# Kernel tuning notes

Hardware: AMD Instinct MI355X
Metric: run time of the kernel (lower is better)

## Reference

```python
import jax, jax.numpy as jnp
import numpy as np

N = 100000   # num entities / tail rows
D_IN = 128
D_OUT = 128
R = 8        # num relations
E = 131072   # edges per relation
B = 32768    # head entities per relation


def setup_inputs() -> dict:
    key = jax.random.key(0)
    ks = jax.random.split(key, 8)
    x = jax.random.normal(ks[0], (N, D_IN), dtype=jnp.float32)
    tail_rep = jax.random.normal(ks[1], (N, D_IN), dtype=jnp.float32)
    # Linear(in, out, bias=False) weight: [out, in], xavier-ish scale
    W = jax.random.normal(ks[2], (D_OUT, D_IN), dtype=jnp.float32) * (1.414 / np.sqrt(D_IN))
    # match_matrix embedding -> per-relation [in, out] matrices
    rel_W = jax.random.normal(ks[3], (R, D_IN, D_OUT), dtype=jnp.float32) * (1.0 / np.sqrt(D_IN))
    edge_weights = jax.random.uniform(ks[4], (R, E), dtype=jnp.float32)
    edge_rows = jax.random.randint(ks[5], (R, E), 0, B, dtype=jnp.int32)
    edge_cols = jax.random.randint(ks[6], (R, E), 0, N, dtype=jnp.int32)
    # head_indice: unique global entity ids per relation (torch code assigns by index)
    rng = np.random.default_rng(0)
    head = np.stack([rng.choice(N, size=B, replace=False) for _ in range(R)]).astype(np.int32)
    head_indice = jnp.asarray(head)
    return {"x": x, "tail_rep": tail_rep, "W": W, "rel_W": rel_W,
            "edge_weights": edge_weights, "edge_rows": edge_rows,
            "edge_cols": edge_cols, "head_indice": head_indice}


def reference(x, tail_rep, W, rel_W, edge_weights, edge_rows, edge_cols, head_indice):
    # emb_all = original_map(input)
    emb_all = x @ W.T                                   # [N, D_OUT]
    # per-relation dense transform of all tails: tail_rep @ rel_W[r]
    transformed = jnp.einsum('ni,rio->rno', tail_rep, rel_W)   # [R, N, D_OUT]
    # sparse.mm(sp_edge_e, all_rep_h): gather tail rows per edge, weight, segment-sum by local head row
    gathered = jnp.take_along_axis(transformed, edge_cols[:, :, None], axis=1)  # [R, E, D_OUT]
    contrib = edge_weights[:, :, None] * gathered                                # [R, E, D_OUT]
    seg = lambda c, rows: jax.ops.segment_sum(c, rows, num_segments=B)
    new_rep = jax.vmap(seg)(contrib, edge_rows)                                  # [R, B, D_OUT]
    # emb_all[ent_indice] = rel_update + emb_all[ent_indice]  (per relation, sequentially) == scatter-add
    emb_all = emb_all.at[head_indice.reshape(-1)].add(new_rep.reshape(-1, D_OUT))
    # activate=True
    return jax.nn.relu(emb_all)
```

## Files before the change

kernel.cpp:

```cpp
#include <hip/hip_runtime.h>
#include <hip/hip_bf16.h>

#define D_DIM 128
#define N_ENT 100000
#define R_REL 8
#define E_EDGE 131072
#define B_HEAD 32768
#define NH_PAD 100352

typedef __attribute__((ext_vector_type(8))) short short8v;
typedef __attribute__((ext_vector_type(16))) float f32x16;

union BF8 {
  short8v v;
  __hip_bfloat16 h[8];
};

__global__ __launch_bounds__(256) void init_ws(int* __restrict__ cnt_e,
                                               int* __restrict__ inv) {
  int i = blockIdx.x * 256 + threadIdx.x;
  if (i < R_REL * B_HEAD) cnt_e[i] = 0;
  inv[i] = -1;
}

__global__ __launch_bounds__(256) void hist_edges(const int* __restrict__ erow,
                                                  int* __restrict__ cnt) {
  int r = blockIdx.y;
  int e = blockIdx.x * 256 + threadIdx.x;
  int row = erow[(size_t)r * E_EDGE + e];
  atomicAdd(cnt + r * B_HEAD + row, 1);
}

__global__ __launch_bounds__(256) void scan_blk(const int* __restrict__ cnt,
                                                int* __restrict__ cur,
                                                int* __restrict__ bsum) {
  int b = blockIdx.x, t = threadIdx.x;
  int4 v = ((const int4*)cnt)[b * 256 + t];
  int s = v.x + v.y + v.z + v.w;
  __shared__ int ps[256];
  ps[t] = s;
  __syncthreads();
  for (int off = 1; off < 256; off <<= 1) {
    int u = (t >= off) ? ps[t - off] : 0;
    __syncthreads();
    ps[t] += u;
    __syncthreads();
  }
  int base = ps[t] - s;
  int4 o;
  o.x = base;
  o.y = base + v.x;
  o.z = o.y + v.y;
  o.w = o.z + v.z;
  ((int4*)cur)[b * 256 + t] = o;
  if (t == 255) bsum[b] = ps[255];
}

__global__ __launch_bounds__(256) void scan_bsum(int* __restrict__ bsum) {
  int t = threadIdx.x;
  int s = bsum[t];
  __shared__ int ps[256];
  ps[t] = s;
  __syncthreads();
  for (int off = 1; off < 256; off <<= 1) {
    int u = (t >= off) ? ps[t - off] : 0;
    __syncthreads();
    ps[t] += u;
    __syncthreads();
  }
  bsum[t] = ps[t] - s;
}

__global__ __launch_bounds__(256) void scan_add(int* __restrict__ cur,
                                                const int* __restrict__ bsum) {
  int i = blockIdx.x * 256 + threadIdx.x;
  int o = bsum[i >> 8];
  int4 v = ((int4*)cur)[i];
  v.x += o; v.y += o; v.z += o; v.w += o;
  ((int4*)cur)[i] = v;
}

__global__ __launch_bounds__(256) void scatter_edges(const int* __restrict__ erow,
                                                     const int* __restrict__ ecol,
                                                     const float* __restrict__ ew,
                                                     int* __restrict__ cur,
                                                     int2* __restrict__ sColW) {
  int r = blockIdx.y;
  int e = blockIdx.x * 256 + threadIdx.x;
  size_t idx = (size_t)r * E_EDGE + e;
  int row = erow[idx];
  int pos = atomicAdd(cur + r * B_HEAD + row, 1);
  sColW[pos] = make_int2(ecol[idx], __float_as_int(ew[idx]));
}

__global__ __launch_bounds__(256) void build_inv(const int* __restrict__ head,
                                                 int* __restrict__ inv) {
  int i = blockIdx.x * 256 + threadIdx.x;
  int r = i >> 15;
  inv[r * NH_PAD + head[i]] = i & (B_HEAD - 1);
}

__global__ __launch_bounds__(256) void csr_agg(const float* __restrict__ tail,
                                               const int* __restrict__ end_e,
                                               const int* __restrict__ cnt_e,
                                               const int2* __restrict__ sColW,
                                               float* __restrict__ agg, int r0) {
  int wid = (blockIdx.x << 2) + (threadIdx.x >> 6);
  int lane = threadIdx.x & 63;
  int f = r0 * B_HEAD + wid;
  int cn = cnt_e[f];
  int s = end_e[f] - cn;
  const float2* tail2 = (const float2*)tail;
  float2 a0 = {0.f, 0.f}, a1 = {0.f, 0.f};
  int k = 0;
  for (; k + 2 <= cn; k += 2) {
    int2 e0 = sColW[s + k];
    int2 e1 = sColW[s + k + 1];
    float2 t0 = tail2[(size_t)e0.x * 64 + lane];
    float2 t1 = tail2[(size_t)e1.x * 64 + lane];
    float w0 = __int_as_float(e0.y), w1 = __int_as_float(e1.y);
    a0.x += w0 * t0.x; a0.y += w0 * t0.y;
    a1.x += w1 * t1.x; a1.y += w1 * t1.y;
  }
  if (k < cn) {
    int2 e0 = sColW[s + k];
    float2 t0 = tail2[(size_t)e0.x * 64 + lane];
    float w0 = __int_as_float(e0.y);
    a0.x += w0 * t0.x; a0.y += w0 * t0.y;
  }
  a0.x += a1.x; a0.y += a1.y;
  ((float2*)agg)[(size_t)wid * 64 + lane] = a0;
}

__global__ __launch_bounds__(256) void prep_W(const float* __restrict__ W,
                                              const float* __restrict__ relW,
                                              short8v* __restrict__ WhS,
                                              short8v* __restrict__ WlS) {
  int mat = blockIdx.y;
  int idx = blockIdx.x * 256 + threadIdx.x;
  int o = idx & 127, ks = idx >> 7;
  float v[8];
  if (mat == 0) {
    const float* src = W + o * D_DIM + ks * 8;
#pragma unroll
    for (int j = 0; j < 8; ++j) v[j] = src[j];
  } else {
    const float* src = relW + (size_t)(mat - 1) * D_DIM * D_DIM + (ks * 8) * D_DIM + o;
#pragma unroll
    for (int j = 0; j < 8; ++j) v[j] = src[j * D_DIM];
  }
  BF8 h, l;
#pragma unroll
  for (int j = 0; j < 8; ++j) {
    __hip_bfloat16 hb = __float2bfloat16(v[j]);
    h.h[j] = hb;
    l.h[j] = __float2bfloat16(v[j] - __bfloat162float(hb));
  }
  WhS[(size_t)mat * 2048 + idx] = h.v;
  WlS[(size_t)mat * 2048 + idx] = l.v;
}

template <bool REL>
__global__ __launch_bounds__(256) void gemm_mfma(const float* __restrict__ Abase,
                                                 const short8v* __restrict__ WhS,
                                                 const short8v* __restrict__ WlS,
                                                 float* __restrict__ Obase, int r0,
                                                 int nrows) {
  __shared__ short8v wlds[2][8][128];
  int tid = threadIdx.x;
  const float* A;
  float* Out;
  int mat;
  if (REL) {
    A = Abase + (size_t)blockIdx.y * B_HEAD * D_DIM;
    Out = Obase + (size_t)blockIdx.y * B_HEAD * D_DIM;
    mat = 1 + r0 + blockIdx.y;
  } else {
    A = Abase;
    Out = Obase;
    mat = 0;
  }
  const short8v* Hsrc = WhS + (size_t)mat * 2048;
  const short8v* Lsrc = WlS + (size_t)mat * 2048;
  int w = tid >> 6, lane = tid & 63, lrow = lane & 31, lsel = lane >> 5;
  int arow = blockIdx.x * 128 + w * 32 + lrow;
  int arowc = (arow < nrows) ? arow : (nrows - 1);
  const float4* Arow = (const float4*)(A + (size_t)arowc * D_DIM);

  f32x16 acc[4] = {};
  for (int half = 0; half < 2; ++half) {
    if (half) __syncthreads();
#pragma unroll
    for (int it = 0; it < 4; ++it) {
      int e = it * 256 + tid;
      wlds[0][e >> 7][e & 127] = Hsrc[half * 1024 + e];
      wlds[1][e >> 7][e & 127] = Lsrc[half * 1024 + e];
    }
    __syncthreads();
#pragma unroll
    for (int kk = 0; kk < 4; ++kk) {
      int k0 = half * 64 + kk * 16;
      float4 a0 = Arow[(k0 >> 2) + lsel * 2];
      float4 a1 = Arow[(k0 >> 2) + lsel * 2 + 1];
      float av[8] = {a0.x, a0.y, a0.z, a0.w, a1.x, a1.y, a1.z, a1.w};
      BF8 ah, al;
#pragma unroll
      for (int j = 0; j < 8; ++j) {
        __hip_bfloat16 hb = __float2bfloat16(av[j]);
        ah.h[j] = hb;
        al.h[j] = __float2bfloat16(av[j] - __bfloat162float(hb));
      }
      int ks = kk * 2 + lsel;
#pragma unroll
      for (int n = 0; n < 4; ++n) {
        short8v bh = wlds[0][ks][n * 32 + lrow];
        short8v bl = wlds[1][ks][n * 32 + lrow];
        acc[n] = __builtin_amdgcn_mfma_f32_32x32x16_bf16(ah.v, bh, acc[n], 0, 0, 0);
        acc[n] = __builtin_amdgcn_mfma_f32_32x32x16_bf16(ah.v, bl, acc[n], 0, 0, 0);
        acc[n] = __builtin_amdgcn_mfma_f32_32x32x16_bf16(al.v, bh, acc[n], 0, 0, 0);
        acc[n] = __builtin_amdgcn_mfma_f32_32x32x16_bf16(al.v, bl, acc[n], 0, 0, 0);
      }
    }
  }
  int wrow0 = blockIdx.x * 128 + w * 32;
#pragma unroll
  for (int reg = 0; reg < 16; ++reg) {
    int srow = wrow0 + (reg & 3) + 8 * (reg >> 2) + 4 * lsel;
    if (srow < nrows) {
      float* orow = Out + (size_t)srow * D_DIM;
#pragma unroll
      for (int n = 0; n < 4; ++n) orow[n * 32 + lrow] = acc[n][reg];
    }
  }
}

__global__ __launch_bounds__(256) void final_add(const int* __restrict__ inv,
                                                 const float* __restrict__ upd,
                                                 float* __restrict__ out, int r0,
                                                 int c, int doRelu) {
  int n = blockIdx.x * 8 + (threadIdx.x >> 5);
  int lane = threadIdx.x & 31;
  if (n >= N_ENT) return;
  float4* o4 = (float4*)out + (size_t)n * 32 + lane;
  float4 v = *o4;
  for (int k = 0; k < c; ++k) {
    int row = inv[(r0 + k) * NH_PAD + n];
    if (row >= 0) {
      const float4* u4 = (const float4*)upd + ((size_t)k * B_HEAD + row) * 32 + lane;
      float4 u = *u4;
      v.x += u.x; v.y += u.y; v.z += u.z; v.w += u.w;
    }
  }
  if (doRelu) {
    v.x = fmaxf(v.x, 0.f); v.y = fmaxf(v.y, 0.f);
    v.z = fmaxf(v.z, 0.f); v.w = fmaxf(v.w, 0.f);
  }
  *o4 = v;
}

extern "C" void kernel_launch(void* const* d_in, const int* in_sizes, int n_in,
                              void* d_out, int out_size, void* d_ws, size_t ws_size,
                              hipStream_t stream) {
  const float* x = (const float*)d_in[0];
  const float* tail = (const float*)d_in[1];
  const float* W = (const float*)d_in[2];
  const float* relW = (const float*)d_in[3];
  const float* ew = (const float*)d_in[4];
  const int* erow = (const int*)d_in[5];
  const int* ecol = (const int*)d_in[6];
  const int* head = (const int*)d_in[7];
  float* out = (float*)d_out;

  char* p = (char*)d_ws;
  short8v* WhS = (short8v*)p; p += (size_t)(R_REL + 1) * 2048 * 16;
  short8v* WlS = (short8v*)p; p += (size_t)(R_REL + 1) * 2048 * 16;
  int* cnt_e = (int*)p;       p += (size_t)R_REL * B_HEAD * 4;
  int* cur_e = (int*)p;       p += (size_t)R_REL * B_HEAD * 4;
  int* inv = (int*)p;         p += (size_t)R_REL * NH_PAD * 4;
  int* bsum = (int*)p;        p += 256 * 4;
  int2* sColW = (int2*)p;     p += (size_t)R_REL * E_EDGE * 8;
  float* agg = (float*)p;
  size_t fixed = (size_t)(p - (char*)d_ws);
  size_t per_rel = (size_t)B_HEAD * D_DIM * 4;
  size_t avail = (ws_size > fixed) ? ws_size - fixed : 0;
  int chunk = (int)(avail / per_rel);
  if (chunk > R_REL) chunk = R_REL;
  if (chunk < 1) chunk = 1;

  init_ws<<<dim3(R_REL * NH_PAD / 256), 256, 0, stream>>>(cnt_e, inv);
  prep_W<<<dim3(8, R_REL + 1), 256, 0, stream>>>(W, relW, WhS, WlS);

  hist_edges<<<dim3(E_EDGE / 256, R_REL), 256, 0, stream>>>(erow, cnt_e);
  scan_blk<<<dim3(256), 256, 0, stream>>>(cnt_e, cur_e, bsum);
  scan_bsum<<<dim3(1), 256, 0, stream>>>(bsum);
  scan_add<<<dim3(256), 256, 0, stream>>>(cur_e, bsum);
  scatter_edges<<<dim3(E_EDGE / 256, R_REL), 256, 0, stream>>>(erow, ecol, ew, cur_e,
                                                               sColW);
  build_inv<<<dim3(R_REL * B_HEAD / 256), 256, 0, stream>>>(head, inv);

  gemm_mfma<false><<<dim3((N_ENT + 127) / 128), 256, 0, stream>>>(x, WhS, WlS, out, 0,
                                                                  N_ENT);

  for (int r0 = 0; r0 < R_REL; r0 += chunk) {
    int c = (R_REL - r0 < chunk) ? (R_REL - r0) : chunk;
    csr_agg<<<dim3(c * B_HEAD / 4), 256, 0, stream>>>(tail, cur_e, cnt_e, sColW, agg,
                                                      r0);
    gemm_mfma<true><<<dim3(B_HEAD / 128, c), 256, 0, stream>>>(agg, WhS, WlS, agg, r0,
                                                               B_HEAD);
    final_add<<<dim3((N_ENT + 7) / 8), 256, 0, stream>>>(inv, agg, out, r0, c,
                                                         (r0 + c == R_REL) ? 1 : 0);
  }
}
```

Baseline: 369.3 us.

## Use bf16 tail/agg/update buffers and fuse scatter-add+relu into x GEMM epilogue

Converts tail_rep to bf16 once so the edge-gather reads half the bytes, stores the aggregated rows and the per-relation transformed updates as bf16, and drops the lo-A split MFMAs in the relation GEMM. When all relations fit in the workspace, the x@W^T GEMM epilogue now gathers all eight relation updates via the inverse index and applies relu, which removes the final_add pass and the extra read-modify-write of the output. The cost is lower precision on the aggregated values, which may push error past tolerance, plus an added conversion kernel that has to read the whole tail matrix.

```diff
diff --git a/kernel.cpp b/kernel.cpp
--- a/kernel.cpp
+++ b/kernel.cpp
@@ -10,17 +10,40 @@
 
 typedef __attribute__((ext_vector_type(8))) short short8v;
 typedef __attribute__((ext_vector_type(16))) float f32x16;
+typedef unsigned int uint;
+typedef unsigned short ushort;
 
 union BF8 {
   short8v v;
   __hip_bfloat16 h[8];
 };
+
+__device__ inline ushort bfbits(float x) {
+  union { __hip_bfloat16 h; ushort u; } c;
+  c.h = __float2bfloat16(x);
+  return c.u;
+}
+__device__ inline float bflo(uint p) { return __uint_as_float(p << 16); }
+__device__ inline float bfhi(uint p) { return __uint_as_float(p & 0xffff0000u); }
 
 __global__ __launch_bounds__(256) void init_ws(int* __restrict__ cnt_e,
                                                int* __restrict__ inv) {
   int i = blockIdx.x * 256 + threadIdx.x;
   if (i < R_REL * B_HEAD) cnt_e[i] = 0;
   inv[i] = -1;
+}
+
+__global__ __launch_bounds__(256) void prep_tail(const float* __restrict__ tail,
+                                                 short8v* __restrict__ tailb) {
+  int i = blockIdx.x * 256 + threadIdx.x;
+  const float4* s = (const float4*)tail + (size_t)i * 2;
+  float4 a = s[0], b = s[1];
+  BF8 h;
+  h.h[0] = __float2bfloat16(a.x); h.h[1] = __float2bfloat16(a.y);
+  h.h[2] = __float2bfloat16(a.z); h.h[3] = __float2bfloat16(a.w);
+  h.h[4] = __float2bfloat16(b.x); h.h[5] = __float2bfloat16(b.y);
+  h.h[6] = __float2bfloat16(b.z); h.h[7] = __float2bfloat16(b.w);
+  tailb[i] = h.v;
 }
 
 __global__ __launch_bounds__(256) void hist_edges(const int* __restrict__ erow,
@@ -48,10 +71,7 @@
   }
   int base = ps[t] - s;
   int4 o;
-  o.x = base;
-  o.y = base + v.x;
-  o.z = o.y + v.y;
-  o.w = o.z + v.z;
+  o.x = base; o.y = base + v.x; o.z = o.y + v.y; o.w = o.z + v.z;
   ((int4*)cur)[b * 256 + t] = o;
   if (t == 255) bsum[b] = ps[255];
 }
@@ -100,36 +120,35 @@
   inv[r * NH_PAD + head[i]] = i & (B_HEAD - 1);
 }
 
-__global__ __launch_bounds__(256) void csr_agg(const float* __restrict__ tail,
+__global__ __launch_bounds__(256) void csr_agg(const uint* __restrict__ tailb,
                                                const int* __restrict__ end_e,
                                                const int* __restrict__ cnt_e,
                                                const int2* __restrict__ sColW,
-                                               float* __restrict__ agg, int r0) {
+                                               uint* __restrict__ aggb, int r0) {
   int wid = (blockIdx.x << 2) + (threadIdx.x >> 6);
   int lane = threadIdx.x & 63;
   int f = r0 * B_HEAD + wid;
   int cn = cnt_e[f];
   int s = end_e[f] - cn;
-  const float2* tail2 = (const float2*)tail;
-  float2 a0 = {0.f, 0.f}, a1 = {0.f, 0.f};
+  float ax = 0.f, ay = 0.f, bx = 0.f, by = 0.f;
   int k = 0;
   for (; k + 2 <= cn; k += 2) {
     int2 e0 = sColW[s + k];
     int2 e1 = sColW[s + k + 1];
-    float2 t0 = tail2[(size_t)e0.x * 64 + lane];
-    float2 t1 = tail2[(size_t)e1.x * 64 + lane];
+    uint t0 = tailb[(size_t)e0.x * 64 + lane];
+    uint t1 = tailb[(size_t)e1.x * 64 + lane];
     float w0 = __int_as_float(e0.y), w1 = __int_as_float(e1.y);
-    a0.x += w0 * t0.x; a0.y += w0 * t0.y;
-    a1.x += w1 * t1.x; a1.y += w1 * t1.y;
+    ax += w0 * bflo(t0); ay += w0 * bfhi(t0);
+    bx += w1 * bflo(t1); by += w1 * bfhi(t1);
   }
   if (k < cn) {
     int2 e0 = sColW[s + k];
-    float2 t0 = tail2[(size_t)e0.x * 64 + lane];
+    uint t0 = tailb[(size_t)e0.x * 64 + lane];
     float w0 = __int_as_float(e0.y);
-    a0.x += w0 * t0.x; a0.y += w0 * t0.y;
-  }
-  a0.x += a1.x; a0.y += a1.y;
-  ((float2*)agg)[(size_t)wid * 64 + lane] = a0;
+    ax += w0 * bflo(t0); ay += w0 * bfhi(t0);
+  }
+  ax += bx; ay += by;
+  aggb[(size_t)wid * 64 + lane] = (uint)bfbits(ax) | ((uint)bfbits(ay) << 16);
 }
 
 __global__ __launch_bounds__(256) void prep_W(const float* __restrict__ W,
@@ -160,32 +179,20 @@
   WlS[(size_t)mat * 2048 + idx] = l.v;
 }
 
-template <bool REL>
-__global__ __launch_bounds__(256) void gemm_mfma(const float* __restrict__ Abase,
-                                                 const short8v* __restrict__ WhS,
-                                                 const short8v* __restrict__ WlS,
-                                                 float* __restrict__ Obase, int r0,
-                                                 int nrows) {
+__global__ __launch_bounds__(256) void gemm_rel(const ushort* __restrict__ aggb,
+                                                const short8v* __restrict__ WhS,
+                                                const short8v* __restrict__ WlS,
+                                                ushort* __restrict__ updb, int r0) {
   __shared__ short8v wlds[2][8][128];
   int tid = threadIdx.x;
-  const float* A;
-  float* Out;
-  int mat;
-  if (REL) {
-    A = Abase + (size_t)blockIdx.y * B_HEAD * D_DIM;
-    Out = Obase + (size_t)blockIdx.y * B_HEAD * D_DIM;
-    mat = 1 + r0 + blockIdx.y;
-  } else {
-    A = Abase;
-    Out = Obase;
-    mat = 0;
-  }
+  int kk_rel = blockIdx.y;
+  int mat = 1 + r0 + kk_rel;
   const short8v* Hsrc = WhS + (size_t)mat * 2048;
   const short8v* Lsrc = WlS + (size_t)mat * 2048;
   int w = tid >> 6, lane = tid & 63, lrow = lane & 31, lsel = lane >> 5;
   int arow = blockIdx.x * 128 + w * 32 + lrow;
-  int arowc = (arow < nrows) ? arow : (nrows - 1);
-  const float4* Arow = (const float4*)(A + (size_t)arowc * D_DIM);
+  const short8v* Arow =
+      (const short8v*)(aggb + ((size_t)kk_rel * B_HEAD + arow) * D_DIM);
 
   f32x16 acc[4] = {};
   for (int half = 0; half < 2; ++half) {
@@ -195,6 +202,53 @@
       int e = it * 256 + tid;
       wlds[0][e >> 7][e & 127] = Hsrc[half * 1024 + e];
       wlds[1][e >> 7][e & 127] = Lsrc[half * 1024 + e];
+    }
+    __syncthreads();
+#pragma unroll
+    for (int kk = 0; kk < 4; ++kk) {
+      short8v a = Arow[half * 8 + kk * 2 + lsel];
+      int ks = kk * 2 + lsel;
+#pragma unroll
+      for (int n = 0; n < 4; ++n) {
+        short8v bh = wlds[0][ks][n * 32 + lrow];
+        short8v bl = wlds[1][ks][n * 32 + lrow];
+        acc[n] = __builtin_amdgcn_mfma_f32_32x32x16_bf16(a, bh, acc[n], 0, 0, 0);
+        acc[n] = __builtin_amdgcn_mfma_f32_32x32x16_bf16(a, bl, acc[n], 0, 0, 0);
+      }
+    }
+  }
+  int wrow0 = blockIdx.x * 128 + w * 32;
+#pragma unroll
+  for (int reg = 0; reg < 16; ++reg) {
+    int srow = wrow0 + (reg & 3) + 8 * (reg >> 2) + 4 * lsel;
+    ushort* urow = updb + ((size_t)kk_rel * B_HEAD + srow) * D_DIM;
+#pragma unroll
+    for (int n = 0; n < 4; ++n) urow[n * 32 + lrow] = bfbits(acc[n][reg]);
+  }
+}
+
+template <bool FUSE>
+__global__ __launch_bounds__(256) void gemm_x(const float* __restrict__ A,
+                                              const short8v* __restrict__ WhS,
+                                              const short8v* __restrict__ WlS,
+                                              const int* __restrict__ inv,
+                                              const ushort* __restrict__ updb,
+                                              float* __restrict__ Out, int nrows) {
+  __shared__ short8v wlds[2][8][128];
+  int tid = threadIdx.x;
+  int w = tid >> 6, lane = tid & 63, lrow = lane & 31, lsel = lane >> 5;
+  int arow = blockIdx.x * 128 + w * 32 + lrow;
+  int arowc = (arow < nrows) ? arow : (nrows - 1);
+  const float4* Arow = (const float4*)(A + (size_t)arowc * D_DIM);
+
+  f32x16 acc[4] = {};
+  for (int half = 0; half < 2; ++half) {
+    if (half) __syncthreads();
+#pragma unroll
+    for (int it = 0; it < 4; ++it) {
+      int e = it * 256 + tid;
+      wlds[0][e >> 7][e & 127] = WhS[half * 1024 + e];
+      wlds[1][e >> 7][e & 127] = WlS[half * 1024 + e];
     }
     __syncthreads();
 #pragma unroll
@@ -227,15 +281,32 @@
   for (int reg = 0; reg < 16; ++reg) {
     int srow = wrow0 + (reg & 3) + 8 * (reg >> 2) + 4 * lsel;
     if (srow < nrows) {
+      float vals[4];
+#pragma unroll
+      for (int n = 0; n < 4; ++n) vals[n] = acc[n][reg];
+      if (FUSE) {
+#pragma unroll
+        for (int r = 0; r < R_REL; ++r) {
+          int row = inv[r * NH_PAD + srow];
+          if (row >= 0) {
+            const ushort* u = updb + ((size_t)r * B_HEAD + row) * D_DIM;
+#pragma unroll
+            for (int n = 0; n < 4; ++n)
+              vals[n] += __uint_as_float((uint)u[n * 32 + lrow] << 16);
+          }
+        }
+#pragma unroll
+        for (int n = 0; n < 4; ++n) vals[n] = fmaxf(vals[n], 0.f);
+      }
       float* orow = Out + (size_t)srow * D_DIM;
 #pragma unroll
-      for (int n = 0; n < 4; ++n) orow[n * 32 + lrow] = acc[n][reg];
+      for (int n = 0; n < 4; ++n) orow[n * 32 + lrow] = vals[n];
     }
   }
 }
 
 __global__ __launch_bounds__(256) void final_add(const int* __restrict__ inv,
-                                                 const float* __restrict__ upd,
+                                                 const ushort* __restrict__ updb,
                                                  float* __restrict__ out, int r0,
                                                  int c, int doRelu) {
   int n = blockIdx.x * 8 + (threadIdx.x >> 5);
@@ -246,9 +317,9 @@
   for (int k = 0; k < c; ++k) {
     int row = inv[(r0 + k) * NH_PAD + n];
     if (row >= 0) {
-      const float4* u4 = (const float4*)upd + ((size_t)k * B_HEAD + row) * 32 + lane;
-      float4 u = *u4;
-      v.x += u.x; v.y += u.y; v.z += u.z; v.w += u.w;
+      uint2 u = ((const uint2*)updb)[((size_t)k * B_HEAD + row) * 32 + lane];
+      v.x += bflo(u.x); v.y += bfhi(u.x);
+      v.z += bflo(u.y); v.w += bfhi(u.y);
     }
   }
   if (doRelu) {
@@ -272,23 +343,27 @@
   float* out = (float*)d_out;
 
   char* p = (char*)d_ws;
-  short8v* WhS = (short8v*)p; p += (size_t)(R_REL + 1) * 2048 * 16;
-  short8v* WlS = (short8v*)p; p += (size_t)(R_REL + 1) * 2048 * 16;
-  int* cnt_e = (int*)p;       p += (size_t)R_REL * B_HEAD * 4;
-  int* cur_e = (int*)p;       p += (size_t)R_REL * B_HEAD * 4;
-  int* inv = (int*)p;         p += (size_t)R_REL * NH_PAD * 4;
-  int* bsum = (int*)p;        p += 256 * 4;
-  int2* sColW = (int2*)p;     p += (size_t)R_REL * E_EDGE * 8;
-  float* agg = (float*)p;
+  short8v* WhS = (short8v*)p;  p += (size_t)(R_REL + 1) * 2048 * 16;
+  short8v* WlS = (short8v*)p;  p += (size_t)(R_REL + 1) * 2048 * 16;
+  short8v* tailb = (short8v*)p; p += (size_t)N_ENT * D_DIM * 2;
+  int* cnt_e = (int*)p;        p += (size_t)R_REL * B_HEAD * 4;
+  int* cur_e = (int*)p;        p += (size_t)R_REL * B_HEAD * 4;
+  int* inv = (int*)p;          p += (size_t)R_REL * NH_PAD * 4;
+  int* bsum = (int*)p;         p += 256 * 4;
+  int2* sColW = (int2*)p;      p += (size_t)R_REL * E_EDGE * 8;
+  char* dyn = p;
   size_t fixed = (size_t)(p - (char*)d_ws);
-  size_t per_rel = (size_t)B_HEAD * D_DIM * 4;
+  size_t per_rel = (size_t)B_HEAD * D_DIM * 2 * 2;
   size_t avail = (ws_size > fixed) ? ws_size - fixed : 0;
   int chunk = (int)(avail / per_rel);
   if (chunk > R_REL) chunk = R_REL;
   if (chunk < 1) chunk = 1;
+  ushort* aggb = (ushort*)dyn;
+  ushort* updb = (ushort*)(dyn + (size_t)chunk * B_HEAD * D_DIM * 2);
 
   init_ws<<<dim3(R_REL * NH_PAD / 256), 256, 0, stream>>>(cnt_e, inv);
   prep_W<<<dim3(8, R_REL + 1), 256, 0, stream>>>(W, relW, WhS, WlS);
+  prep_tail<<<dim3(N_ENT * D_DIM / 8 / 256), 256, 0, stream>>>(tail, tailb);
 
   hist_edges<<<dim3(E_EDGE / 256, R_REL), 256, 0, stream>>>(erow, cnt_e);
   scan_blk<<<dim3(256), 256, 0, stream>>>(cnt_e, cur_e, bsum);
@@ -298,16 +373,22 @@
                                                                sColW);
   build_inv<<<dim3(R_REL * B_HEAD / 256), 256, 0, stream>>>(head, inv);
 
-  gemm_mfma<false><<<dim3((N_ENT + 127) / 128), 256, 0, stream>>>(x, WhS, WlS, out, 0,
-                                                                  N_ENT);
-
-  for (int r0 = 0; r0 < R_REL; r0 += chunk) {
-    int c = (R_REL - r0 < chunk) ? (R_REL - r0) : chunk;
-    csr_agg<<<dim3(c * B_HEAD / 4), 256, 0, stream>>>(tail, cur_e, cnt_e, sColW, agg,
-                                                      r0);
-    gemm_mfma<true><<<dim3(B_HEAD / 128, c), 256, 0, stream>>>(agg, WhS, WlS, agg, r0,
-                                                               B_HEAD);
-    final_add<<<dim3((N_ENT + 7) / 8), 256, 0, stream>>>(inv, agg, out, r0, c,
-                                                         (r0 + c == R_REL) ? 1 : 0);
-  }
-}
+  if (chunk == R_REL) {
+    csr_agg<<<dim3(R_REL * B_HEAD / 4), 256, 0, stream>>>(
+        (const uint*)tailb, cur_e, cnt_e, sColW, (uint*)aggb, 0);
+    gemm_rel<<<dim3(B_HEAD / 128, R_REL), 256, 0, stream>>>(aggb, WhS, WlS, updb, 0);
+    gemm_x<true><<<dim3((N_ENT + 127) / 128), 256, 0, stream>>>(x, WhS, WlS, inv,
+                                                                updb, out, N_ENT);
+  } else {
+    gemm_x<false><<<dim3((N_ENT + 127) / 128), 256, 0, stream>>>(x, WhS, WlS, inv,
+                                                                 updb, out, N_ENT);
+    for (int r0 = 0; r0 < R_REL; r0 += chunk) {
+      int c = (R_REL - r0 < chunk) ? (R_REL - r0) : chunk;
+      csr_agg<<<dim3(c * B_HEAD / 4), 256, 0, stream>>>(
+          (const uint*)tailb, cur_e, cnt_e, sColW, (uint*)aggb, r0);
+      gemm_rel<<<dim3(B_HEAD / 128, c), 256, 0, stream>>>(aggb, WhS, WlS, updb, r0);
+      final_add<<<dim3((N_ENT + 7) / 8), 256, 0, stream>>>(inv, updb, out, r0, c,
+                                                           (r0 + c == R_REL) ? 1 : 0);
+    }
+  }
+}
```

Result: slower. 387.0 us (+4.8%).
